# Kernel tuning notes

Hardware: AMD Instinct MI355X
Metric: run time of the kernel (lower is better)

## Reference

```python
import jax, jax.numpy as jnp
import numpy as np

N_NODES = 100000


def gcn_conv(x, src, dst, w, W, b, n):
    # PyG GCNConv: add self loops (weight 1), symmetric normalization,
    # linear transform, scatter-add aggregation, bias.
    loop = jnp.arange(n, dtype=src.dtype)
    s = jnp.concatenate([src, loop])
    d = jnp.concatenate([dst, loop])
    ew = jnp.concatenate([w, jnp.ones((n,), dtype=w.dtype)])
    deg = jax.ops.segment_sum(ew, d, num_segments=n)          # [N]
    dinv = jnp.where(deg > 0, jax.lax.rsqrt(deg), 0.0).astype(x.dtype)
    norm = dinv[s] * ew * dinv[d]                             # [E+N]
    h = x @ W                                                 # [N, out]
    msg = h[s] * norm[:, None]                                # gather + scale
    out = jax.ops.segment_sum(msg, d, num_segments=n)         # scatter-add
    return out + b


def setup_inputs() -> dict:
    key = jax.random.key(0)
    k1, k2, k3, k4, k5, k6 = jax.random.split(key, 6)
    n, e, c_in, c_hid, c_out = N_NODES, 1200000, 64, 64, 32
    node_matrix = jax.random.normal(k1, (n, c_in), dtype=jnp.float32)
    edge_index = jax.random.randint(k2, (2, e), 0, n, dtype=jnp.int64)
    edge_weights = jax.random.uniform(k3, (e,), dtype=jnp.float32)
    s_in = 1.0 / np.sqrt(c_in)
    s_hid = 1.0 / np.sqrt(c_hid)
    W1 = jax.random.uniform(k4, (c_in, c_hid), jnp.float32, -s_in, s_in)
    b1 = jnp.zeros((c_hid,), jnp.float32)
    W2 = jax.random.uniform(k5, (c_hid, c_out), jnp.float32, -s_hid, s_hid)
    b2 = jnp.zeros((c_out,), jnp.float32)
    return {"node_matrix": node_matrix, "edge_index": edge_index,
            "edge_weights": edge_weights, "W1": W1, "b1": b1, "W2": W2, "b2": b2}


def reference(node_matrix, edge_index, edge_weights, W1, b1, W2, b2):
    n = node_matrix.shape[0]
    src, dst = edge_index[0], edge_index[1]
    x = gcn_conv(node_matrix, src, dst, edge_weights, W1, b1, n)
    x = jax.nn.relu(x)
    x = gcn_conv(x, src, dst, edge_weights, W2, b2, n)
    return x
```

## Files before the change

kernel.cpp:

```cpp
#include <hip/hip_runtime.h>

static inline int ceil_div(long long a, long long b) { return (int)((a + b - 1) / b); }

#define RBITS 8
#define RNODES 256
#define CAPB 12
#define CAP 4096

typedef __attribute__((ext_vector_type(8))) short bf16x8;
typedef __attribute__((ext_vector_type(4))) float f32x4;
typedef __attribute__((ext_vector_type(2))) unsigned u32x2;
typedef __attribute__((ext_vector_type(4))) unsigned u32x4;

__device__ inline unsigned f2bf(float f) {
    unsigned u = __float_as_uint(f);
    return (u + 0x7fffu + ((u >> 16) & 1u)) >> 16;
}
__device__ inline unsigned pack2(float a, float b) { return f2bf(a) | (f2bf(b) << 16); }
__device__ inline float bf2f(unsigned v) { return __uint_as_float(v << 16); }
__device__ inline float bf_lo(unsigned v) { return __uint_as_float(v << 16); }
__device__ inline float bf_hi(unsigned v) { return __uint_as_float(v & 0xffff0000u); }

#define SC_T 512
#define SC_K 8
#define SC_E (SC_T * SC_K)
__global__ void bin_scatter(const int* __restrict__ src, const int* __restrict__ dst,
                            const float* __restrict__ w, int* __restrict__ bin_cursor,
                            int* __restrict__ bp, float* __restrict__ bw,
                            int NB, int E) {
    __shared__ int hist[512];
    __shared__ int offs[512];
    __shared__ int base[512];
    __shared__ int stage_p[SC_E];
    __shared__ float stage_w[SC_E];
    __shared__ unsigned short stage_b[SC_E];
    int t = threadIdx.x;
    hist[t] = 0;
    __syncthreads();
    int e0 = blockIdx.x * SC_E;
    int nE = E - e0; if (nE > SC_E) nE = SC_E;

    int myBin[SC_K], myRank[SC_K], myPack[SC_K];
    float myW[SC_K];
#pragma unroll
    for (int k = 0; k < SC_K; ++k) {
        int idx = t + k * SC_T;
        if (idx < nE) {
            int e = e0 + idx;
            int d = dst[e];
            int b = d >> RBITS;
            myBin[k] = b;
            myPack[k] = (src[e] << RBITS) | (d & (RNODES - 1));
            myW[k] = w[e];
            myRank[k] = atomicAdd(&hist[b], 1);
        }
    }
    __syncthreads();
    offs[t] = hist[t];
    __syncthreads();
    for (int d = 1; d < 512; d <<= 1) {
        int a = (t >= d) ? offs[t - d] : 0;
        __syncthreads();
        offs[t] += a;
        __syncthreads();
    }
    if (t < NB && hist[t]) base[t] = (t << CAPB) + atomicAdd(&bin_cursor[t], hist[t]);
#pragma unroll
    for (int k = 0; k < SC_K; ++k) {
        int idx = t + k * SC_T;
        if (idx < nE) {
            int b = myBin[k];
            int pos = (offs[b] - hist[b]) + myRank[k];
            stage_p[pos] = myPack[k];
            stage_w[pos] = myW[k];
            stage_b[pos] = (unsigned short)b;
        }
    }
    __syncthreads();
    for (int p = t; p < nE; p += SC_T) {
        int b = stage_b[p];
        int g = base[b] + (p - (offs[b] - hist[b]));
        bp[g] = stage_p[p];
        bw[g] = stage_w[p];
    }
}

__global__ void build_csr(const int* __restrict__ bp, const float* __restrict__ bw,
                          const int* __restrict__ bin_len,
                          unsigned* __restrict__ row_rc, float* __restrict__ dinv,
                          u32x2* __restrict__ ew, int N) {
    __shared__ int bp_s[CAP];
    __shared__ float bw_s[CAP];
    __shared__ int cnt[RNODES];
    __shared__ float wsum[RNODES];
    __shared__ int starts[RNODES];
    __shared__ int cur[RNODES];
    int b = blockIdx.x;
    int t = threadIdx.x;
    int len = bin_len[b];
    int base = b << CAPB;
    if (t < RNODES) { cnt[t] = 0; wsum[t] = 0.f; }
    __syncthreads();
    for (int e = t; e < len; e += 512) {
        int p = bp[base + e];
        float wv = bw[base + e];
        bp_s[e] = p;
        bw_s[e] = wv;
        atomicAdd(&cnt[p & (RNODES - 1)], 1);
        atomicAdd(&wsum[p & (RNODES - 1)], wv);
    }
    __syncthreads();
    if (t < RNODES) starts[t] = cnt[t];
    __syncthreads();
    for (int d = 1; d < RNODES; d <<= 1) {
        int a = 0;
        if (t < RNODES && t >= d) a = starts[t - d];
        __syncthreads();
        if (t < RNODES) starts[t] += a;
        __syncthreads();
    }
    if (t < RNODES) {
        int s0 = starts[t] - cnt[t];
        cur[t] = s0;
        int node = (b << RBITS) + t;
        if (node < N) {
            row_rc[node] = (unsigned)(base + s0) | ((unsigned)cnt[t] << 21);
            dinv[node] = rsqrtf(wsum[t] + 1.0f);
        }
    }
    __syncthreads();
    for (int e = t; e < len; e += 512) {
        int p = bp_s[e];
        int slot = atomicAdd(&cur[p & (RNODES - 1)], 1);
        u32x2 v;
        v.x = (unsigned)(p >> RBITS);
        v.y = __float_as_uint(bw_s[e]);
        ew[base + slot] = v;
    }
}

__global__ __launch_bounds__(256) void gemm1_mfma(const float* __restrict__ X,
                                                  const float* __restrict__ W,
                                                  const float* __restrict__ dinv,
                                                  unsigned short* __restrict__ H, int N) {
    int lane = threadIdx.x & 63;
    int wv = threadIdx.x >> 6;
    int quad = lane >> 4;
    int col = lane & 15;

    bf16x8 Bh[4][2], Bl[4][2];
#pragma unroll
    for (int nt = 0; nt < 4; ++nt)
#pragma unroll
        for (int kh = 0; kh < 2; ++kh)
#pragma unroll
            for (int j = 0; j < 8; ++j) {
                float wval = W[(kh * 32 + quad * 8 + j) * 64 + nt * 16 + col];
                unsigned hb = f2bf(wval);
                Bh[nt][kh][j] = (short)hb;
                Bl[nt][kh][j] = (short)f2bf(wval - bf2f(hb));
            }

#pragma unroll
    for (int rt = 0; rt < 4; ++rt) {
        int rb = blockIdx.x * 256 + wv * 64 + rt * 16;
        if (rb >= N) break;
        int arow = rb + col;
        bf16x8 Ah[2], Al[2];
#pragma unroll
        for (int kh = 0; kh < 2; ++kh) {
            float xv[8];
            if (arow < N) {
                const float4* p = (const float4*)(X + (size_t)arow * 64 + kh * 32 + quad * 8);
                float4 f0 = p[0], f1 = p[1];
                xv[0] = f0.x; xv[1] = f0.y; xv[2] = f0.z; xv[3] = f0.w;
                xv[4] = f1.x; xv[5] = f1.y; xv[6] = f1.z; xv[7] = f1.w;
            } else {
#pragma unroll
                for (int j = 0; j < 8; ++j) xv[j] = 0.f;
            }
#pragma unroll
            for (int j = 0; j < 8; ++j) {
                unsigned hb = f2bf(xv[j]);
                Ah[kh][j] = (short)hb;
                Al[kh][j] = (short)f2bf(xv[j] - bf2f(hb));
            }
        }
        f32x4 acc[4] = {{0,0,0,0},{0,0,0,0},{0,0,0,0},{0,0,0,0}};
#pragma unroll
        for (int nt = 0; nt < 4; ++nt)
#pragma unroll
            for (int kh = 0; kh < 2; ++kh) {
                acc[nt] = __builtin_amdgcn_mfma_f32_16x16x32_bf16(Ah[kh], Bh[nt][kh], acc[nt], 0, 0, 0);
                acc[nt] = __builtin_amdgcn_mfma_f32_16x16x32_bf16(Al[kh], Bh[nt][kh], acc[nt], 0, 0, 0);
                acc[nt] = __builtin_amdgcn_mfma_f32_16x16x32_bf16(Ah[kh], Bl[nt][kh], acc[nt], 0, 0, 0);
            }
        float di[4];
#pragma unroll
        for (int r = 0; r < 4; ++r) {
            int row = rb + quad * 4 + r;
            di[r] = (row < N) ? dinv[row] : 0.f;
        }
#pragma unroll
        for (int nt = 0; nt < 4; ++nt)
#pragma unroll
            for (int r = 0; r < 4; ++r) {
                int row = rb + quad * 4 + r;
                if (row < N)
                    H[(size_t)row * 64 + nt * 16 + col] = (unsigned short)f2bf(di[r] * acc[nt][r]);
            }
    }
}

__global__ __launch_bounds__(256) void gemm2_mfma(const unsigned short* __restrict__ Xb,
                                                  const float* __restrict__ W,
                                                  const float* __restrict__ dinv,
                                                  unsigned short* __restrict__ H, int N) {
    int lane = threadIdx.x & 63;
    int wv = threadIdx.x >> 6;
    int quad = lane >> 4;
    int col = lane & 15;

    bf16x8 Bh[2][2], Bl[2][2];
#pragma unroll
    for (int nt = 0; nt < 2; ++nt)
#pragma unroll
        for (int kh = 0; kh < 2; ++kh)
#pragma unroll
            for (int j = 0; j < 8; ++j) {
                float wval = W[(kh * 32 + quad * 8 + j) * 32 + nt * 16 + col];
                unsigned hb = f2bf(wval);
                Bh[nt][kh][j] = (short)hb;
                Bl[nt][kh][j] = (short)f2bf(wval - bf2f(hb));
            }

#pragma unroll
    for (int rt = 0; rt < 4; ++rt) {
        int rb = blockIdx.x * 256 + wv * 64 + rt * 16;
        if (rb >= N) break;
        int arow = rb + col;
        bf16x8 A[2];
#pragma unroll
        for (int kh = 0; kh < 2; ++kh) {
            if (arow < N) {
                const bf16x8* p = (const bf16x8*)(Xb + (size_t)arow * 64 + kh * 32 + quad * 8);
                A[kh] = *p;
            } else {
                A[kh] = bf16x8{0,0,0,0,0,0,0,0};
            }
        }
        f32x4 acc[2] = {{0,0,0,0},{0,0,0,0}};
#pragma unroll
        for (int nt = 0; nt < 2; ++nt)
#pragma unroll
            for (int kh = 0; kh < 2; ++kh) {
                acc[nt] = __builtin_amdgcn_mfma_f32_16x16x32_bf16(A[kh], Bh[nt][kh], acc[nt], 0, 0, 0);
                acc[nt] = __builtin_amdgcn_mfma_f32_16x16x32_bf16(A[kh], Bl[nt][kh], acc[nt], 0, 0, 0);
            }
        float di[4];
#pragma unroll
        for (int r = 0; r < 4; ++r) {
            int row = rb + quad * 4 + r;
            di[r] = (row < N) ? dinv[row] : 0.f;
        }
#pragma unroll
        for (int nt = 0; nt < 2; ++nt)
#pragma unroll
            for (int r = 0; r < 4; ++r) {
                int row = rb + quad * 4 + r;
                if (row < N)
                    H[(size_t)row * 32 + nt * 16 + col] = (unsigned short)f2bf(di[r] * acc[nt][r]);
            }
    }
}

__global__ void aggregate64(const unsigned* __restrict__ h, const unsigned* __restrict__ row_rc,
                            const u32x2* __restrict__ ew, const float* __restrict__ dinv,
                            const float* __restrict__ b, unsigned* __restrict__ outb, int N) {
    int t = threadIdx.x;
    int c = t & 7;
    int i = blockIdx.x * 64 + (t >> 3);
    if (i >= N) return;
    unsigned rc = row_rc[i];
    int e = (int)(rc & 0x1FFFFFu);
    int end = e + (int)(rc >> 21);
    const uint4* h4 = (const uint4*)h;
    float acc[8];
#pragma unroll
    for (int j = 0; j < 8; ++j) acc[j] = 0.f;
    for (; e + 3 < end; e += 4) {
        u32x2 e0 = __builtin_nontemporal_load(&ew[e]);
        u32x2 e1 = __builtin_nontemporal_load(&ew[e + 1]);
        u32x2 e2 = __builtin_nontemporal_load(&ew[e + 2]);
        u32x2 e3 = __builtin_nontemporal_load(&ew[e + 3]);
        float n0 = __uint_as_float(e0.y);
        float n1 = __uint_as_float(e1.y);
        float n2 = __uint_as_float(e2.y);
        float n3 = __uint_as_float(e3.y);
        uint4 v0 = h4[(size_t)e0.x * 8 + c];
        uint4 v1 = h4[(size_t)e1.x * 8 + c];
        uint4 v2 = h4[(size_t)e2.x * 8 + c];
        uint4 v3 = h4[(size_t)e3.x * 8 + c];
        acc[0] += n0 * bf_lo(v0.x) + n1 * bf_lo(v1.x) + n2 * bf_lo(v2.x) + n3 * bf_lo(v3.x);
        acc[1] += n0 * bf_hi(v0.x) + n1 * bf_hi(v1.x) + n2 * bf_hi(v2.x) + n3 * bf_hi(v3.x);
        acc[2] += n0 * bf_lo(v0.y) + n1 * bf_lo(v1.y) + n2 * bf_lo(v2.y) + n3 * bf_lo(v3.y);
        acc[3] += n0 * bf_hi(v0.y) + n1 * bf_hi(v1.y) + n2 * bf_hi(v2.y) + n3 * bf_hi(v3.y);
        acc[4] += n0 * bf_lo(v0.z) + n1 * bf_lo(v1.z) + n2 * bf_lo(v2.z) + n3 * bf_lo(v3.z);
        acc[5] += n0 * bf_hi(v0.z) + n1 * bf_hi(v1.z) + n2 * bf_hi(v2.z) + n3 * bf_hi(v3.z);
        acc[6] += n0 * bf_lo(v0.w) + n1 * bf_lo(v1.w) + n2 * bf_lo(v2.w) + n3 * bf_lo(v3.w);
        acc[7] += n0 * bf_hi(v0.w) + n1 * bf_hi(v1.w) + n2 * bf_hi(v2.w) + n3 * bf_hi(v3.w);
    }
    for (; e < end; ++e) {
        u32x2 e0 = __builtin_nontemporal_load(&ew[e]);
        float n0 = __uint_as_float(e0.y);
        uint4 v0 = h4[(size_t)e0.x * 8 + c];
        acc[0] += n0 * bf_lo(v0.x);
        acc[1] += n0 * bf_hi(v0.x);
        acc[2] += n0 * bf_lo(v0.y);
        acc[3] += n0 * bf_hi(v0.y);
        acc[4] += n0 * bf_lo(v0.z);
        acc[5] += n0 * bf_hi(v0.z);
        acc[6] += n0 * bf_lo(v0.w);
        acc[7] += n0 * bf_hi(v0.w);
    }
    float di = dinv[i];
    uint4 hv = h4[(size_t)i * 8 + c];
    float hs[8] = {bf_lo(hv.x), bf_hi(hv.x), bf_lo(hv.y), bf_hi(hv.y),
                   bf_lo(hv.z), bf_hi(hv.z), bf_lo(hv.w), bf_hi(hv.w)};
    float4 b0 = ((const float4*)b)[c * 2];
    float4 b1 = ((const float4*)b)[c * 2 + 1];
    float o[8];
    o[0] = b0.x + di * (hs[0] + acc[0]);
    o[1] = b0.y + di * (hs[1] + acc[1]);
    o[2] = b0.z + di * (hs[2] + acc[2]);
    o[3] = b0.w + di * (hs[3] + acc[3]);
    o[4] = b1.x + di * (hs[4] + acc[4]);
    o[5] = b1.y + di * (hs[5] + acc[5]);
    o[6] = b1.z + di * (hs[6] + acc[6]);
    o[7] = b1.w + di * (hs[7] + acc[7]);
#pragma unroll
    for (int j = 0; j < 8; ++j) o[j] = fmaxf(o[j], 0.f);
    u32x4 ov;
    ov.x = pack2(o[0], o[1]);
    ov.y = pack2(o[2], o[3]);
    ov.z = pack2(o[4], o[5]);
    ov.w = pack2(o[6], o[7]);
    __builtin_nontemporal_store(ov, (u32x4*)outb + (size_t)i * 8 + c);
}

__global__ void aggregate32(const unsigned* __restrict__ h, const unsigned* __restrict__ row_rc,
                            const u32x2* __restrict__ ew, const float* __restrict__ dinv,
                            const float* __restrict__ b, float* __restrict__ out, int N) {
    int t = threadIdx.x;
    int c = t & 3;
    int i = blockIdx.x * 128 + (t >> 2);
    if (i >= N) return;
    unsigned rc = row_rc[i];
    int e = (int)(rc & 0x1FFFFFu);
    int end = e + (int)(rc >> 21);
    const uint4* h4 = (const uint4*)h;
    float acc[8];
#pragma unroll
    for (int j = 0; j < 8; ++j) acc[j] = 0.f;
    for (; e + 3 < end; e += 4) {
        u32x2 e0 = __builtin_nontemporal_load(&ew[e]);
        u32x2 e1 = __builtin_nontemporal_load(&ew[e + 1]);
        u32x2 e2 = __builtin_nontemporal_load(&ew[e + 2]);
        u32x2 e3 = __builtin_nontemporal_load(&ew[e + 3]);
        float n0 = __uint_as_float(e0.y);
        float n1 = __uint_as_float(e1.y);
        float n2 = __uint_as_float(e2.y);
        float n3 = __uint_as_float(e3.y);
        uint4 v0 = h4[(size_t)e0.x * 4 + c];
        uint4 v1 = h4[(size_t)e1.x * 4 + c];
        uint4 v2 = h4[(size_t)e2.x * 4 + c];
        uint4 v3 = h4[(size_t)e3.x * 4 + c];
        acc[0] += n0 * bf_lo(v0.x) + n1 * bf_lo(v1.x) + n2 * bf_lo(v2.x) + n3 * bf_lo(v3.x);
        acc[1] += n0 * bf_hi(v0.x) + n1 * bf_hi(v1.x) + n2 * bf_hi(v2.x) + n3 * bf_hi(v3.x);
        acc[2] += n0 * bf_lo(v0.y) + n1 * bf_lo(v1.y) + n2 * bf_lo(v2.y) + n3 * bf_lo(v3.y);
        acc[3] += n0 * bf_hi(v0.y) + n1 * bf_hi(v1.y) + n2 * bf_hi(v2.y) + n3 * bf_hi(v3.y);
        acc[4] += n0 * bf_lo(v0.z) + n1 * bf_lo(v1.z) + n2 * bf_lo(v2.z) + n3 * bf_lo(v3.z);
        acc[5] += n0 * bf_hi(v0.z) + n1 * bf_hi(v1.z) + n2 * bf_hi(v2.z) + n3 * bf_hi(v3.z);
        acc[6] += n0 * bf_lo(v0.w) + n1 * bf_lo(v1.w) + n2 * bf_lo(v2.w) + n3 * bf_lo(v3.w);
        acc[7] += n0 * bf_hi(v0.w) + n1 * bf_hi(v1.w) + n2 * bf_hi(v2.w) + n3 * bf_hi(v3.w);
    }
    for (; e < end; ++e) {
        u32x2 e0 = __builtin_nontemporal_load(&ew[e]);
        float n0 = __uint_as_float(e0.y);
        uint4 v0 = h4[(size_t)e0.x * 4 + c];
        acc[0] += n0 * bf_lo(v0.x);
        acc[1] += n0 * bf_hi(v0.x);
        acc[2] += n0 * bf_lo(v0.y);
        acc[3] += n0 * bf_hi(v0.y);
        acc[4] += n0 * bf_lo(v0.z);
        acc[5] += n0 * bf_hi(v0.z);
        acc[6] += n0 * bf_lo(v0.w);
        acc[7] += n0 * bf_hi(v0.w);
    }
    float di = dinv[i];
    uint4 hv = h4[(size_t)i * 4 + c];
    float hs[8] = {bf_lo(hv.x), bf_hi(hv.x), bf_lo(hv.y), bf_hi(hv.y),
                   bf_lo(hv.z), bf_hi(hv.z), bf_lo(hv.w), bf_hi(hv.w)};
    float4 b0 = ((const float4*)b)[c * 2];
    float4 b1 = ((const float4*)b)[c * 2 + 1];
    f32x4 o0, o1;
    o0.x = b0.x + di * (hs[0] + acc[0]);
    o0.y = b0.y + di * (hs[1] + acc[1]);
    o0.z = b0.z + di * (hs[2] + acc[2]);
    o0.w = b0.w + di * (hs[3] + acc[3]);
    o1.x = b1.x + di * (hs[4] + acc[4]);
    o1.y = b1.y + di * (hs[5] + acc[5]);
    o1.z = b1.z + di * (hs[6] + acc[6]);
    o1.w = b1.w + di * (hs[7] + acc[7]);
    f32x4* op = (f32x4*)(out + (size_t)i * 32 + c * 8);
    __builtin_nontemporal_store(o0, op);
    __builtin_nontemporal_store(o1, op + 1);
}

extern "C" void kernel_launch(void* const* d_in, const int* in_sizes, int n_in,
                              void* d_out, int out_size, void* d_ws, size_t ws_size,
                              hipStream_t stream) {
    const float* x  = (const float*)d_in[0];
    const int* eidx = (const int*)d_in[1];
    const float* w  = (const float*)d_in[2];
    const float* W1 = (const float*)d_in[3];
    const float* b1 = (const float*)d_in[4];
    const float* W2 = (const float*)d_in[5];
    const float* b2 = (const float*)d_in[6];
    float* out = (float*)d_out;

    const int E = in_sizes[2];
    const int N = in_sizes[0] / 64;
    const int* src = eidx;
    const int* dst = eidx + E;
    const int NB = ceil_div(N, RNODES);

    char* ws = (char*)d_ws;
    size_t off = 0;
    auto alloc = [&](size_t bytes) -> void* {
        void* p = ws + off;
        off = (off + bytes + 255) & ~(size_t)255;
        return p;
    };
    int*      bin_cursor = (int*)alloc((size_t)NB * 4);
    int*      bp         = (int*)alloc((size_t)NB * CAP * 4);
    float*    bw         = (float*)alloc((size_t)NB * CAP * 4);
    u32x2*    ew         = (u32x2*)alloc((size_t)NB * CAP * 8);
    unsigned* row_rc     = (unsigned*)alloc((size_t)N * 4);
    float*    dinv       = (float*)alloc((size_t)N * 4);
    unsigned* h1         = (unsigned*)alloc((size_t)N * 32 * 4);
    unsigned* out1b      = (unsigned*)alloc((size_t)N * 32 * 4);
    unsigned* h2         = (unsigned*)alloc((size_t)N * 16 * 4);

    (void)hipMemsetAsync(bin_cursor, 0, (size_t)NB * 4, stream);
    bin_scatter<<<ceil_div(E, SC_E), SC_T, 0, stream>>>(src, dst, w, bin_cursor, bp, bw, NB, E);
    build_csr<<<NB, 512, 0, stream>>>(bp, bw, bin_cursor, row_rc, dinv, ew, N);

    gemm1_mfma<<<ceil_div(N, 256), 256, 0, stream>>>(x, W1, dinv, (unsigned short*)h1, N);
    aggregate64<<<ceil_div(N, 64), 512, 0, stream>>>(h1, row_rc, ew, dinv, b1, out1b, N);

    gemm2_mfma<<<ceil_div(N, 256), 256, 0, stream>>>((const unsigned short*)out1b, W2, dinv,
                                                     (unsigned short*)h2, N);
    aggregate32<<<ceil_div(N, 128), 512, 0, stream>>>(h2, row_rc, ew, dinv, b2, out, N);
}
```

Measured before the change: 213.0 us.

## Sort CSR edges by coarse source segment and drop nontemporal hints

```diff
diff --git a/kernel.cpp b/kernel.cpp
--- a/kernel.cpp
+++ b/kernel.cpp
@@ -6,6 +6,9 @@
 #define RNODES 256
 #define CAPB 12
 #define CAP 4096
+#define SEGB 15
+#define SEGS 4
+#define NKEY (RNODES * SEGS)
 
 typedef __attribute__((ext_vector_type(8))) short bf16x8;
 typedef __attribute__((ext_vector_type(4))) float f32x4;
@@ -91,47 +94,57 @@
                           u32x2* __restrict__ ew, int N) {
     __shared__ int bp_s[CAP];
     __shared__ float bw_s[CAP];
-    __shared__ int cnt[RNODES];
+    __shared__ int cnt[NKEY];
+    __shared__ int starts[NKEY];
+    __shared__ int cur[NKEY];
     __shared__ float wsum[RNODES];
-    __shared__ int starts[RNODES];
-    __shared__ int cur[RNODES];
     int b = blockIdx.x;
     int t = threadIdx.x;
     int len = bin_len[b];
     int base = b << CAPB;
-    if (t < RNODES) { cnt[t] = 0; wsum[t] = 0.f; }
+    for (int k = t; k < NKEY; k += 512) cnt[k] = 0;
+    if (t < RNODES) wsum[t] = 0.f;
     __syncthreads();
     for (int e = t; e < len; e += 512) {
         int p = bp[base + e];
         float wv = bw[base + e];
         bp_s[e] = p;
         bw_s[e] = wv;
-        atomicAdd(&cnt[p & (RNODES - 1)], 1);
-        atomicAdd(&wsum[p & (RNODES - 1)], wv);
-    }
-    __syncthreads();
-    if (t < RNODES) starts[t] = cnt[t];
-    __syncthreads();
-    for (int d = 1; d < RNODES; d <<= 1) {
-        int a = 0;
-        if (t < RNODES && t >= d) a = starts[t - d];
+        int off = p & (RNODES - 1);
+        int seg = (p >> RBITS) >> SEGB;
+        atomicAdd(&cnt[off * SEGS + seg], 1);
+        atomicAdd(&wsum[off], wv);
+    }
+    __syncthreads();
+    starts[t] = cnt[t];
+    starts[t + 512] = cnt[t + 512];
+    __syncthreads();
+    for (int d = 1; d < NKEY; d <<= 1) {
+        int j0 = t, j1 = t + 512;
+        int a0 = (j0 >= d) ? starts[j0 - d] : 0;
+        int a1 = (j1 >= d) ? starts[j1 - d] : 0;
         __syncthreads();
-        if (t < RNODES) starts[t] += a;
+        starts[j0] += a0;
+        starts[j1] += a1;
         __syncthreads();
     }
+    for (int k = t; k < NKEY; k += 512) cur[k] = starts[k] - cnt[k];
+    __syncthreads();
     if (t < RNODES) {
-        int s0 = starts[t] - cnt[t];
-        cur[t] = s0;
+        int s0 = starts[t * SEGS] - cnt[t * SEGS];
+        int rcnt = starts[t * SEGS + SEGS - 1] - s0;
         int node = (b << RBITS) + t;
         if (node < N) {
-            row_rc[node] = (unsigned)(base + s0) | ((unsigned)cnt[t] << 21);
+            row_rc[node] = (unsigned)(base + s0) | ((unsigned)rcnt << 21);
             dinv[node] = rsqrtf(wsum[t] + 1.0f);
         }
     }
     __syncthreads();
     for (int e = t; e < len; e += 512) {
         int p = bp_s[e];
-        int slot = atomicAdd(&cur[p & (RNODES - 1)], 1);
+        int off = p & (RNODES - 1);
+        int seg = (p >> RBITS) >> SEGB;
+        int slot = atomicAdd(&cur[off * SEGS + seg], 1);
         u32x2 v;
         v.x = (unsigned)(p >> RBITS);
         v.y = __float_as_uint(bw_s[e]);
@@ -289,10 +302,7 @@
 #pragma unroll
     for (int j = 0; j < 8; ++j) acc[j] = 0.f;
     for (; e + 3 < end; e += 4) {
-        u32x2 e0 = __builtin_nontemporal_load(&ew[e]);
-        u32x2 e1 = __builtin_nontemporal_load(&ew[e + 1]);
-        u32x2 e2 = __builtin_nontemporal_load(&ew[e + 2]);
-        u32x2 e3 = __builtin_nontemporal_load(&ew[e + 3]);
+        u32x2 e0 = ew[e], e1 = ew[e + 1], e2 = ew[e + 2], e3 = ew[e + 3];
         float n0 = __uint_as_float(e0.y);
         float n1 = __uint_as_float(e1.y);
         float n2 = __uint_as_float(e2.y);
@@ -311,7 +321,7 @@
         acc[7] += n0 * bf_hi(v0.w) + n1 * bf_hi(v1.w) + n2 * bf_hi(v2.w) + n3 * bf_hi(v3.w);
     }
     for (; e < end; ++e) {
-        u32x2 e0 = __builtin_nontemporal_load(&ew[e]);
+        u32x2 e0 = ew[e];
         float n0 = __uint_as_float(e0.y);
         uint4 v0 = h4[(size_t)e0.x * 8 + c];
         acc[0] += n0 * bf_lo(v0.x);
@@ -340,12 +350,12 @@
     o[7] = b1.w + di * (hs[7] + acc[7]);
 #pragma unroll
     for (int j = 0; j < 8; ++j) o[j] = fmaxf(o[j], 0.f);
-    u32x4 ov;
+    uint4 ov;
     ov.x = pack2(o[0], o[1]);
     ov.y = pack2(o[2], o[3]);
     ov.z = pack2(o[4], o[5]);
     ov.w = pack2(o[6], o[7]);
-    __builtin_nontemporal_store(ov, (u32x4*)outb + (size_t)i * 8 + c);
+    ((uint4*)outb)[(size_t)i * 8 + c] = ov;
 }
 
 __global__ void aggregate32(const unsigned* __restrict__ h, const unsigned* __restrict__ row_rc,
@@ -363,10 +373,7 @@
 #pragma unroll
     for (int j = 0; j < 8; ++j) acc[j] = 0.f;
     for (; e + 3 < end; e += 4) {
-        u32x2 e0 = __builtin_nontemporal_load(&ew[e]);
-        u32x2 e1 = __builtin_nontemporal_load(&ew[e + 1]);
-        u32x2 e2 = __builtin_nontemporal_load(&ew[e + 2]);
-        u32x2 e3 = __builtin_nontemporal_load(&ew[e + 3]);
+        u32x2 e0 = ew[e], e1 = ew[e + 1], e2 = ew[e + 2], e3 = ew[e + 3];
         float n0 = __uint_as_float(e0.y);
         float n1 = __uint_as_float(e1.y);
         float n2 = __uint_as_float(e2.y);
@@ -385,7 +392,7 @@
         acc[7] += n0 * bf_hi(v0.w) + n1 * bf_hi(v1.w) + n2 * bf_hi(v2.w) + n3 * bf_hi(v3.w);
     }
     for (; e < end; ++e) {
-        u32x2 e0 = __builtin_nontemporal_load(&ew[e]);
+        u32x2 e0 = ew[e];
         float n0 = __uint_as_float(e0.y);
         uint4 v0 = h4[(size_t)e0.x * 4 + c];
         acc[0] += n0 * bf_lo(v0.x);
```

Result: faster. 203.2 us (-4.6%).
